# Performance work log

Hardware: AMD Instinct MI355X
Metric: run time of the kernel (lower is better)

The kernel has to match this reference:

```python
import jax, jax.numpy as jnp
import numpy as np

EPS = 1e-5
NUM_HEAD = 8
HEAD_DIM = 64
SCALE = HEAD_DIM ** -0.5


def setup_inputs() -> dict:
    key = jax.random.key(0)
    ks = jax.random.split(key, 3)
    b, n, dim = 4, 2048, 512
    inner = NUM_HEAD * HEAD_DIM  # 512
    x = jax.random.normal(ks[0], (b, n, dim), dtype=jnp.float32)
    ln_w = jnp.ones((dim,), jnp.float32)
    ln_b = jnp.zeros((dim,), jnp.float32)
    qkv_w = jax.random.normal(ks[1], (3 * inner, dim), jnp.float32) * (dim ** -0.5)
    qkv_b = jnp.zeros((3 * inner,), jnp.float32)
    out_w = jax.random.normal(ks[2], (dim, inner), jnp.float32) * (inner ** -0.5)
    out_b = jnp.zeros((dim,), jnp.float32)
    return {"x": x, "ln_w": ln_w, "ln_b": ln_b, "qkv_w": qkv_w,
            "qkv_b": qkv_b, "out_w": out_w, "out_b": out_b}


def reference(x, ln_w, ln_b, qkv_w, qkv_b, out_w, out_b):
    b, n, dim = x.shape
    # Pre-norm LayerNorm
    mu = jnp.mean(x, axis=-1, keepdims=True)
    var = jnp.mean(jnp.square(x - mu), axis=-1, keepdims=True)
    xn = (x - mu) * jax.lax.rsqrt(var + EPS) * ln_w + ln_b
    # QKV projection (torch Linear: y = x @ W.T + b)
    qkv = xn @ qkv_w.T + qkv_b  # [b, n, 3*inner]
    q, k, v = jnp.split(qkv, 3, axis=-1)
    def heads(t):  # [b, n, inner] -> [b, h, n, d]
        return t.reshape(b, n, NUM_HEAD, HEAD_DIM).transpose(0, 2, 1, 3)
    q, k, v = heads(q), heads(k), heads(v)
    # Naive full attention (materializes [b, h, n, n])
    dots = jnp.einsum('bhqd,bhkd->bhqk', q, k) * SCALE
    attn = jax.nn.softmax(dots, axis=-1)
    o = jnp.einsum('bhqk,bhkd->bhqd', attn, v)
    o = o.transpose(0, 2, 1, 3).reshape(b, n, NUM_HEAD * HEAD_DIM)
    return o @ out_w.T + out_b
```

## Files before the change

kernel.cpp:

```cpp
#include <hip/hip_runtime.h>

typedef __attribute__((ext_vector_type(8))) short bf16x8;
typedef __attribute__((ext_vector_type(4))) float floatx4;

#define B_    4
#define N_    2048
#define DIM_  512
#define NH_   8
#define HD_   64
#define SCALE_ 0.125f
#define SL2E_ (0.125f * 1.44269504f)

__device__ __forceinline__ unsigned short f32_to_bf16(float f) {
    unsigned int u = __float_as_uint(f);
    u += 0x7FFFu + ((u >> 16) & 1u);
    return (unsigned short)(u >> 16);
}

__device__ __forceinline__ float bf16_to_f32(unsigned short u) {
    return __uint_as_float(((unsigned int)u) << 16);
}

__device__ __forceinline__ floatx4 mfma16(bf16x8 a, bf16x8 b, floatx4 c) {
    return __builtin_amdgcn_mfma_f32_16x16x32_bf16(a, b, c, 0, 0, 0);
}

__device__ __forceinline__ floatx4 fzero4() {
    floatx4 z = {0.f, 0.f, 0.f, 0.f};
    return z;
}

__device__ __forceinline__ void async16(const unsigned short* g, unsigned short* l) {
    __builtin_amdgcn_global_load_lds((const __attribute__((address_space(1))) void*)g,
                                     (__attribute__((address_space(3))) void*)l,
                                     16, 0, 0);
}

__global__ __launch_bounds__(256) void ln_kernel(const float* __restrict__ x,
                                                 const float* __restrict__ w,
                                                 const float* __restrict__ b,
                                                 unsigned short* __restrict__ xn) {
    int row = blockIdx.x;
    int tid = threadIdx.x;
    int lane = tid & 63, wid = tid >> 6;
    const float2 v = ((const float2*)(x + (size_t)row * DIM_))[tid];
    float s = v.x + v.y;
    float sq = v.x * v.x + v.y * v.y;
#pragma unroll
    for (int off = 1; off < 64; off <<= 1) {
        s  += __shfl_xor(s, off, 64);
        sq += __shfl_xor(sq, off, 64);
    }
    __shared__ float red[2][4];
    if (lane == 0) { red[0][wid] = s; red[1][wid] = sq; }
    __syncthreads();
    s  = red[0][0] + red[0][1] + red[0][2] + red[0][3];
    sq = red[1][0] + red[1][1] + red[1][2] + red[1][3];
    float mu   = s * (1.f / DIM_);
    float var  = sq * (1.f / DIM_) - mu * mu;
    float rstd = rsqrtf(var + 1e-5f);
    float2 wv = ((const float2*)w)[tid];
    float2 bv = ((const float2*)b)[tid];
    float y0 = (v.x - mu) * rstd * wv.x + bv.x;
    float y1 = (v.y - mu) * rstd * wv.y + bv.y;
    unsigned int pack = (unsigned int)f32_to_bf16(y0) |
                        ((unsigned int)f32_to_bf16(y1) << 16);
    ((unsigned int*)xn)[(size_t)row * (DIM_ / 2) + tid] = pack;
}

__global__ __launch_bounds__(256) void cvt_kernel(const float* __restrict__ srcA, int na,
                                                  const float* __restrict__ srcB, int nb,
                                                  unsigned short* __restrict__ dstA,
                                                  unsigned short* __restrict__ dstB) {
    int idx = blockIdx.x * 256 + threadIdx.x;
    if (idx < na)            dstA[idx] = f32_to_bf16(srcA[idx]);
    else if (idx < na + nb)  dstB[idx - na] = f32_to_bf16(srcB[idx - na]);
}

#define GEMM_CORE(A_, B_ptr, am0, bn0)                                              \
    __shared__ unsigned short Alds[2][128][32];                                     \
    __shared__ unsigned short Blds[2][128][32];                                     \
    int tid = threadIdx.x, lane = tid & 63, wid = tid >> 6;                         \
    int l15 = lane & 15, quad = lane >> 4;                                          \
    int wmloc = (wid >> 1) * 64, wnloc = (wid & 1) * 64;                            \
    int sr = lane >> 2;                                                             \
    int sc = (lane & 3) * 8;                                                        \
    floatx4 acc[4][4];                                                              \
    _Pragma("unroll")                                                               \
    for (int i = 0; i < 4; i++)                                                     \
        _Pragma("unroll")                                                           \
        for (int j = 0; j < 4; j++) acc[i][j] = fzero4();                           \
    int buf = 0;                                                                    \
    _Pragma("unroll")                                                               \
    for (int i = 0; i < 2; i++) {                                                   \
        int r0 = 32 * wid + 16 * i;                                                 \
        async16(A_ + (size_t)(am0 + r0 + sr) * DIM_ + sc, &Alds[0][r0][0]);         \
        async16(B_ptr + (size_t)(bn0 + r0 + sr) * DIM_ + sc, &Blds[0][r0][0]);      \
    }                                                                               \
    __syncthreads();                                                                \
    for (int t = 0; t < 16; t++) {                                                  \
        if (t < 15) {                                                               \
            int k0 = (t + 1) * 32;                                                  \
            _Pragma("unroll")                                                       \
            for (int i = 0; i < 2; i++) {                                           \
                int r0 = 32 * wid + 16 * i;                                         \
                async16(A_ + (size_t)(am0 + r0 + sr) * DIM_ + k0 + sc,              \
                        &Alds[buf ^ 1][r0][0]);                                     \
                async16(B_ptr + (size_t)(bn0 + r0 + sr) * DIM_ + k0 + sc,           \
                        &Blds[buf ^ 1][r0][0]);                                     \
            }                                                                       \
        }                                                                           \
        bf16x8 av[4], bv[4];                                                        \
        _Pragma("unroll")                                                           \
        for (int i = 0; i < 4; i++)                                                 \
            av[i] = *(const bf16x8*)(&Alds[buf][wmloc + 16 * i + l15][quad * 8]);   \
        _Pragma("unroll")                                                           \
        for (int j = 0; j < 4; j++)                                                 \
            bv[j] = *(const bf16x8*)(&Blds[buf][wnloc + 16 * j + l15][quad * 8]);   \
        _Pragma("unroll")                                                           \
        for (int i = 0; i < 4; i++)                                                 \
            _Pragma("unroll")                                                       \
            for (int j = 0; j < 4; j++)                                             \
                acc[i][j] = mfma16(av[i], bv[j], acc[i][j]);                        \
        __syncthreads();                                                            \
        buf ^= 1;                                                                   \
    }

__global__ __launch_bounds__(256, 4) void qkv_gemm(const unsigned short* __restrict__ A,
                                                   const unsigned short* __restrict__ Bw,
                                                   const float* __restrict__ bias,
                                                   unsigned short* __restrict__ Qh,
                                                   unsigned short* __restrict__ Kh,
                                                   unsigned short* __restrict__ Vt) {
    int am0 = blockIdx.x * 128, bn0 = blockIdx.y * 128;
    GEMM_CORE(A, Bw, am0, bn0)

    if (bn0 >= 1024) {
        unsigned short* sc_ = &Alds[0][0][0] + wid * (16 * 68);
        int m0 = am0 + wmloc;
        int bidx = m0 >> 11;
        int t0 = m0 & 2047;
#pragma unroll
        for (int j = 0; j < 4; j++) {
            float bias_n = bias[bn0 + wnloc + 16 * j + l15];
#pragma unroll
            for (int i = 0; i < 4; i++)
#pragma unroll
                for (int r = 0; r < 4; r++)
                    sc_[l15 * 68 + 16 * i + quad * 4 + r] =
                        f32_to_bf16(acc[i][j][r] + bias_n);
#pragma unroll
            for (int half = 0; half < 2; half++) {
                int nr = 8 * half + (lane >> 3);
                int rem = (bn0 - 1024) + wnloc + 16 * j + nr;
                int head = rem >> 6, d = rem & 63;
                bf16x8 vv = *(const bf16x8*)(sc_ + nr * 68 + (lane & 7) * 8);
                *(bf16x8*)(Vt + ((size_t)(bidx * NH_ + head) * HD_ + d) * N_ +
                           t0 + (lane & 7) * 8) = vv;
            }
        }
    } else {
#pragma unroll
        for (int i = 0; i < 4; i++) {
#pragma unroll
            for (int j = 0; j < 4; j++) {
                int n = bn0 + wnloc + 16 * j + l15;
                float bias_n = bias[n];
                int which = n >> 9;
                int rem = n & 511;
                int head = rem >> 6;
                int d = rem & 63;
#pragma unroll
                for (int r = 0; r < 4; r++) {
                    int m = am0 + wmloc + 16 * i + quad * 4 + r;
                    int b = m >> 11;
                    int t = m & 2047;
                    float val = acc[i][j][r] + bias_n;
                    if (which == 0) {
                        Qh[((size_t)(b * NH_ + head) * N_ + t) * HD_ + d] =
                            f32_to_bf16(val * SL2E_);
                    } else {
                        Kh[((size_t)(b * NH_ + head) * N_ + t) * HD_ + d] =
                            f32_to_bf16(val);
                    }
                }
            }
        }
    }
}

__global__ __launch_bounds__(256, 4) void out_gemm(const unsigned short* __restrict__ A,
                                                   const unsigned short* __restrict__ Bw,
                                                   const float* __restrict__ bias,
                                                   float* __restrict__ out) {
    int am0 = blockIdx.x * 128, bn0 = blockIdx.y * 128;
    GEMM_CORE(A, Bw, am0, bn0)

#pragma unroll
    for (int i = 0; i < 4; i++) {
#pragma unroll
        for (int j = 0; j < 4; j++) {
            int n = bn0 + wnloc + 16 * j + l15;
            float bias_n = bias[n];
#pragma unroll
            for (int r = 0; r < 4; r++) {
                int m = am0 + wmloc + 16 * i + quad * 4 + r;
                out[(size_t)m * DIM_ + n] = acc[i][j][r] + bias_n;
            }
        }
    }
}

__global__ __launch_bounds__(256, 4) void attn_kernel(const unsigned short* __restrict__ Qh,
                                                      const unsigned short* __restrict__ Kh,
                                                      const unsigned short* __restrict__ Vtg,
                                                      unsigned short* __restrict__ Opart,
                                                      float* __restrict__ lpart) {
    int bh = blockIdx.y;
    int b = bh >> 3, head = bh & 7;
    int qt = blockIdx.x;
    int split = blockIdx.z;
    int kv0 = split << 10;
    int tid = threadIdx.x, lane = tid & 63, w = tid >> 6;
    int l15 = lane & 15, quad = lane >> 4;

    const unsigned short* Qp = Qh + (size_t)bh * N_ * HD_;
    const unsigned short* Kg = Kh + (size_t)bh * N_ * HD_;
    const unsigned short* Vg = Vtg + (size_t)bh * HD_ * N_;

    int q0 = qt * 128 + w * 32;

    bf16x8 aQ[2][2];
#pragma unroll
    for (int mh = 0; mh < 2; mh++) {
        const unsigned short* qrow = Qp + (size_t)(q0 + mh * 16 + l15) * HD_ + quad * 8;
        aQ[mh][0] = *(const bf16x8*)(qrow);
        aQ[mh][1] = *(const bf16x8*)(qrow + 32);
    }

    floatx4 of[2][4];
#pragma unroll
    for (int mh = 0; mh < 2; mh++)
#pragma unroll
        for (int t = 0; t < 4; t++) of[mh][t] = fzero4();
    floatx4 lacc[2];
    lacc[0] = fzero4(); lacc[1] = fzero4();

    const short onebf = (short)0x3F80;
    bf16x8 ones = {onebf, onebf, onebf, onebf, onebf, onebf, onebf, onebf};

    __shared__ unsigned short Kt[64][64];
    __shared__ unsigned short Vs[64][64];
    __shared__ unsigned short Pl[4][32][72];

    int srow = lane >> 3;
    int scol = ((lane & 7) ^ srow) * 8;

    int swz0 = (quad ^ (l15 & 7)) * 8;
    int swz1 = ((quad + 4) ^ (l15 & 7)) * 8;

    unsigned short* myP = &Pl[w][0][0];
    for (int kv = kv0; kv < kv0 + 1024; kv += 64) {
#pragma unroll
        for (int i = 0; i < 2; i++) {
            int r0 = 16 * w + 8 * i;
            async16(Kg + (size_t)(kv + r0 + srow) * HD_ + scol, &Kt[r0][0]);
            async16(Vg + (size_t)(r0 + srow) * N_ + kv + scol, &Vs[r0][0]);
        }
        __syncthreads();
        bf16x8 kf[8];
#pragma unroll
        for (int h = 0; h < 4; h++) {
            kf[2 * h]     = *(const bf16x8*)(&Kt[16 * h + l15][swz0]);
            kf[2 * h + 1] = *(const bf16x8*)(&Kt[16 * h + l15][swz1]);
        }
#pragma unroll
        for (int mh = 0; mh < 2; mh++) {
            floatx4 c[4];
#pragma unroll
            for (int h = 0; h < 4; h++) {
                floatx4 cc = fzero4();
                cc = mfma16(aQ[mh][0], kf[2 * h], cc);
                cc = mfma16(aQ[mh][1], kf[2 * h + 1], cc);
                c[h] = cc;
            }
            unsigned short* pw = myP + (mh * 16 + quad * 4) * 72 + l15;
#pragma unroll
            for (int h = 0; h < 4; h++)
#pragma unroll
                for (int r = 0; r < 4; r++)
                    pw[r * 72 + h * 16] = f32_to_bf16(exp2f(c[h][r]));
        }
        bf16x8 vf[8];
#pragma unroll
        for (int t = 0; t < 4; t++) {
            vf[2 * t]     = *(const bf16x8*)(&Vs[16 * t + l15][swz0]);
            vf[2 * t + 1] = *(const bf16x8*)(&Vs[16 * t + l15][swz1]);
        }
#pragma unroll
        for (int mh = 0; mh < 2; mh++) {
            const unsigned short* pr = myP + (mh * 16 + l15) * 72;
            bf16x8 aP0 = *(const bf16x8*)(pr + quad * 8);
            bf16x8 aP1 = *(const bf16x8*)(pr + 32 + quad * 8);
#pragma unroll
            for (int t = 0; t < 4; t++) {
                of[mh][t] = mfma16(aP0, vf[2 * t], of[mh][t]);
                of[mh][t] = mfma16(aP1, vf[2 * t + 1], of[mh][t]);
            }
            lacc[mh] = mfma16(aP0, ones, lacc[mh]);
            lacc[mh] = mfma16(aP1, ones, lacc[mh]);
        }
        __syncthreads();
    }

    unsigned short* Od = Opart + (size_t)split * B_ * N_ * DIM_;
#pragma unroll
    for (int mh = 0; mh < 2; mh++) {
        float inv[4];
#pragma unroll
        for (int r = 0; r < 4; r++) inv[r] = 1.f / lacc[mh][r];
#pragma unroll
        for (int t = 0; t < 4; t++) {
#pragma unroll
            for (int r = 0; r < 4; r++) {
                int t_tok = q0 + mh * 16 + quad * 4 + r;
                int d = 16 * t + l15;
                Od[((size_t)b * N_ + t_tok) * DIM_ + head * HD_ + d] =
                    f32_to_bf16(of[mh][t][r] * inv[r]);
            }
        }
        if (l15 == 0) {
#pragma unroll
            for (int r = 0; r < 4; r++) {
                int t_tok = q0 + mh * 16 + quad * 4 + r;
                lpart[(size_t)split * B_ * NH_ * N_ + (size_t)bh * N_ + t_tok] =
                    lacc[mh][r];
            }
        }
    }
}

__global__ __launch_bounds__(256) void combine_kernel(const unsigned short* __restrict__ Opart,
                                                      const float* __restrict__ lpart,
                                                      unsigned short* __restrict__ Obuf) {
    int idx = blockIdx.x * 256 + threadIdx.x;
    int row = idx >> 7;
    int head = (idx & 127) >> 4;
    int b = row >> 11, t = row & 2047;
    size_t li = (size_t)(b * NH_ + head) * N_ + t;
    float l1 = lpart[li];
    float l2 = lpart[(size_t)B_ * NH_ * N_ + li];
    float s = 1.f / (l1 + l2);
    float w1 = l1 * s, w2 = l2 * s;
    const size_t half = (size_t)B_ * N_ * DIM_;
    ushort4 a = ((const ushort4*)Opart)[idx];
    ushort4 c = ((const ushort4*)(Opart + half))[idx];
    ushort4 o;
    o.x = f32_to_bf16(w1 * bf16_to_f32(a.x) + w2 * bf16_to_f32(c.x));
    o.y = f32_to_bf16(w1 * bf16_to_f32(a.y) + w2 * bf16_to_f32(c.y));
    o.z = f32_to_bf16(w1 * bf16_to_f32(a.z) + w2 * bf16_to_f32(c.z));
    o.w = f32_to_bf16(w1 * bf16_to_f32(a.w) + w2 * bf16_to_f32(c.w));
    ((ushort4*)Obuf)[idx] = o;
}

extern "C" void kernel_launch(void* const* d_in, const int* in_sizes, int n_in,
                              void* d_out, int out_size, void* d_ws, size_t ws_size,
                              hipStream_t stream) {
    const float* x     = (const float*)d_in[0];
    const float* ln_w  = (const float*)d_in[1];
    const float* ln_b  = (const float*)d_in[2];
    const float* qkv_w = (const float*)d_in[3];
    const float* qkv_b = (const float*)d_in[4];
    const float* out_w = (const float*)d_in[5];
    const float* out_b = (const float*)d_in[6];
    float* out = (float*)d_out;

    char* ws = (char*)d_ws;
    const size_t TOK = (size_t)B_ * N_;
    unsigned short* xn    = (unsigned short*)ws;  ws += TOK * DIM_ * 2;
    unsigned short* wq_bf = (unsigned short*)ws;  ws += (size_t)3 * DIM_ * DIM_ * 2;
    unsigned short* wo_bf = (unsigned short*)ws;  ws += (size_t)DIM_ * DIM_ * 2;
    unsigned short* Qh    = (unsigned short*)ws;  ws += TOK * DIM_ * 2;
    unsigned short* Kh    = (unsigned short*)ws;  ws += TOK * DIM_ * 2;
    unsigned short* Vt    = (unsigned short*)ws;  ws += TOK * DIM_ * 2;
    unsigned short* Obuf  = (unsigned short*)ws;  ws += TOK * DIM_ * 2;
    unsigned short* Opart = (unsigned short*)ws;  ws += (size_t)2 * TOK * DIM_ * 2;
    float*          lpart = (float*)ws;           ws += (size_t)2 * B_ * NH_ * N_ * 4;

    const int NW = 3 * DIM_ * DIM_;
    const int NO = DIM_ * DIM_;

    ln_kernel<<<TOK, 256, 0, stream>>>(x, ln_w, ln_b, xn);
    cvt_kernel<<<(NW + NO + 255) / 256, 256, 0, stream>>>(qkv_w, NW, out_w, NO, wq_bf, wo_bf);
    qkv_gemm<<<dim3(TOK / 128, (3 * DIM_) / 128), 256, 0, stream>>>(xn, wq_bf, qkv_b, Qh, Kh, Vt);
    attn_kernel<<<dim3(N_ / 128, B_ * NH_, 2), 256, 0, stream>>>(Qh, Kh, Vt, Opart, lpart);
    combine_kernel<<<(TOK * DIM_) / 4 / 256, 256, 0, stream>>>(Opart, lpart, Obuf);
    out_gemm<<<dim3(TOK / 128, DIM_ / 128), 256, 0, stream>>>(Obuf, wo_bf, out_b, out);
}
```

Before: 183.0 us.

## Use 512-thread GEMM blocks and four-way KV split in attention

The QKV and output GEMMs move to 512-thread blocks, with each of eight waves computing a 32x64 sub-tile, so more waves are available to hide latency. The attention kernel splits the KV range into four chunks instead of two, which doubles the grid. It also processes P and V per 16-row half to shrink the P shared-memory buffer and reduce register pressure, with a higher occupancy hint. The combine kernel now merges four partials, which adds extra global traffic for Opart and lpart.

```diff
diff --git a/kernel.cpp b/kernel.cpp
--- a/kernel.cpp
+++ b/kernel.cpp
@@ -77,48 +77,41 @@
     else if (idx < na + nb)  dstB[idx - na] = f32_to_bf16(srcB[idx - na]);
 }
 
-#define GEMM_CORE(A_, B_ptr, am0, bn0)                                              \
+#define GEMM_CORE512(A_, B_ptr, am0, bn0)                                           \
     __shared__ unsigned short Alds[2][128][32];                                     \
     __shared__ unsigned short Blds[2][128][32];                                     \
     int tid = threadIdx.x, lane = tid & 63, wid = tid >> 6;                         \
     int l15 = lane & 15, quad = lane >> 4;                                          \
-    int wmloc = (wid >> 1) * 64, wnloc = (wid & 1) * 64;                            \
+    int wmloc = (wid >> 1) * 32, wnloc = (wid & 1) * 64;                            \
     int sr = lane >> 2;                                                             \
     int sc = (lane & 3) * 8;                                                        \
-    floatx4 acc[4][4];                                                              \
+    int srow0 = 16 * wid;                                                           \
+    floatx4 acc[2][4];                                                              \
     _Pragma("unroll")                                                               \
-    for (int i = 0; i < 4; i++)                                                     \
+    for (int i = 0; i < 2; i++)                                                     \
         _Pragma("unroll")                                                           \
         for (int j = 0; j < 4; j++) acc[i][j] = fzero4();                           \
     int buf = 0;                                                                    \
-    _Pragma("unroll")                                                               \
-    for (int i = 0; i < 2; i++) {                                                   \
-        int r0 = 32 * wid + 16 * i;                                                 \
-        async16(A_ + (size_t)(am0 + r0 + sr) * DIM_ + sc, &Alds[0][r0][0]);         \
-        async16(B_ptr + (size_t)(bn0 + r0 + sr) * DIM_ + sc, &Blds[0][r0][0]);      \
-    }                                                                               \
+    async16(A_ + (size_t)(am0 + srow0 + sr) * DIM_ + sc, &Alds[0][srow0][0]);       \
+    async16(B_ptr + (size_t)(bn0 + srow0 + sr) * DIM_ + sc, &Blds[0][srow0][0]);    \
     __syncthreads();                                                                \
     for (int t = 0; t < 16; t++) {                                                  \
         if (t < 15) {                                                               \
             int k0 = (t + 1) * 32;                                                  \
-            _Pragma("unroll")                                                       \
-            for (int i = 0; i < 2; i++) {                                           \
-                int r0 = 32 * wid + 16 * i;                                         \
-                async16(A_ + (size_t)(am0 + r0 + sr) * DIM_ + k0 + sc,              \
-                        &Alds[buf ^ 1][r0][0]);                                     \
-                async16(B_ptr + (size_t)(bn0 + r0 + sr) * DIM_ + k0 + sc,           \
-                        &Blds[buf ^ 1][r0][0]);                                     \
-            }                                                                       \
+            async16(A_ + (size_t)(am0 + srow0 + sr) * DIM_ + k0 + sc,               \
+                    &Alds[buf ^ 1][srow0][0]);                                      \
+            async16(B_ptr + (size_t)(bn0 + srow0 + sr) * DIM_ + k0 + sc,            \
+                    &Blds[buf ^ 1][srow0][0]);                                      \
         }                                                                           \
-        bf16x8 av[4], bv[4];                                                        \
+        bf16x8 av[2], bv[4];                                                        \
         _Pragma("unroll")                                                           \
-        for (int i = 0; i < 4; i++)                                                 \
+        for (int i = 0; i < 2; i++)                                                 \
             av[i] = *(const bf16x8*)(&Alds[buf][wmloc + 16 * i + l15][quad * 8]);   \
         _Pragma("unroll")                                                           \
         for (int j = 0; j < 4; j++)                                                 \
             bv[j] = *(const bf16x8*)(&Blds[buf][wnloc + 16 * j + l15][quad * 8]);   \
         _Pragma("unroll")                                                           \
-        for (int i = 0; i < 4; i++)                                                 \
+        for (int i = 0; i < 2; i++)                                                 \
             _Pragma("unroll")                                                       \
             for (int j = 0; j < 4; j++)                                             \
                 acc[i][j] = mfma16(av[i], bv[j], acc[i][j]);                        \
@@ -126,17 +119,17 @@
         buf ^= 1;                                                                   \
     }
 
-__global__ __launch_bounds__(256, 4) void qkv_gemm(const unsigned short* __restrict__ A,
+__global__ __launch_bounds__(512, 6) void qkv_gemm(const unsigned short* __restrict__ A,
                                                    const unsigned short* __restrict__ Bw,
                                                    const float* __restrict__ bias,
                                                    unsigned short* __restrict__ Qh,
                                                    unsigned short* __restrict__ Kh,
                                                    unsigned short* __restrict__ Vt) {
     int am0 = blockIdx.x * 128, bn0 = blockIdx.y * 128;
-    GEMM_CORE(A, Bw, am0, bn0)
+    GEMM_CORE512(A, Bw, am0, bn0)
 
     if (bn0 >= 1024) {
-        unsigned short* sc_ = &Alds[0][0][0] + wid * (16 * 68);
+        unsigned short* sc_ = &Alds[0][0][0] + wid * (16 * 40);
         int m0 = am0 + wmloc;
         int bidx = m0 >> 11;
         int t0 = m0 & 2047;
@@ -144,24 +137,21 @@
         for (int j = 0; j < 4; j++) {
             float bias_n = bias[bn0 + wnloc + 16 * j + l15];
 #pragma unroll
-            for (int i = 0; i < 4; i++)
+            for (int i = 0; i < 2; i++)
 #pragma unroll
                 for (int r = 0; r < 4; r++)
-                    sc_[l15 * 68 + 16 * i + quad * 4 + r] =
+                    sc_[l15 * 40 + 16 * i + quad * 4 + r] =
                         f32_to_bf16(acc[i][j][r] + bias_n);
-#pragma unroll
-            for (int half = 0; half < 2; half++) {
-                int nr = 8 * half + (lane >> 3);
-                int rem = (bn0 - 1024) + wnloc + 16 * j + nr;
-                int head = rem >> 6, d = rem & 63;
-                bf16x8 vv = *(const bf16x8*)(sc_ + nr * 68 + (lane & 7) * 8);
-                *(bf16x8*)(Vt + ((size_t)(bidx * NH_ + head) * HD_ + d) * N_ +
-                           t0 + (lane & 7) * 8) = vv;
-            }
+            int nr = lane >> 2;
+            int rem = (bn0 - 1024) + wnloc + 16 * j + nr;
+            int head = rem >> 6, d = rem & 63;
+            bf16x8 vv = *(const bf16x8*)(sc_ + nr * 40 + (lane & 3) * 8);
+            *(bf16x8*)(Vt + ((size_t)(bidx * NH_ + head) * HD_ + d) * N_ +
+                       t0 + (lane & 3) * 8) = vv;
         }
     } else {
 #pragma unroll
-        for (int i = 0; i < 4; i++) {
+        for (int i = 0; i < 2; i++) {
 #pragma unroll
             for (int j = 0; j < 4; j++) {
                 int n = bn0 + wnloc + 16 * j + l15;
@@ -189,15 +179,15 @@
     }
 }
 
-__global__ __launch_bounds__(256, 4) void out_gemm(const unsigned short* __restrict__ A,
+__global__ __launch_bounds__(512, 4) void out_gemm(const unsigned short* __restrict__ A,
                                                    const unsigned short* __restrict__ Bw,
                                                    const float* __restrict__ bias,
                                                    float* __restrict__ out) {
     int am0 = blockIdx.x * 128, bn0 = blockIdx.y * 128;
-    GEMM_CORE(A, Bw, am0, bn0)
-
-#pragma unroll
-    for (int i = 0; i < 4; i++) {
+    GEMM_CORE512(A, Bw, am0, bn0)
+
+#pragma unroll
+    for (int i = 0; i < 2; i++) {
 #pragma unroll
         for (int j = 0; j < 4; j++) {
             int n = bn0 + wnloc + 16 * j + l15;
@@ -211,7 +201,7 @@
     }
 }
 
-__global__ __launch_bounds__(256, 4) void attn_kernel(const unsigned short* __restrict__ Qh,
+__global__ __launch_bounds__(256, 6) void attn_kernel(const unsigned short* __restrict__ Qh,
                                                       const unsigned short* __restrict__ Kh,
                                                       const unsigned short* __restrict__ Vtg,
                                                       unsigned short* __restrict__ Opart,
@@ -220,7 +210,7 @@
     int b = bh >> 3, head = bh & 7;
     int qt = blockIdx.x;
     int split = blockIdx.z;
-    int kv0 = split << 10;
+    int kv0 = split << 9;
     int tid = threadIdx.x, lane = tid & 63, w = tid >> 6;
     int l15 = lane & 15, quad = lane >> 4;
 
@@ -251,7 +241,7 @@
 
     __shared__ unsigned short Kt[64][64];
     __shared__ unsigned short Vs[64][64];
-    __shared__ unsigned short Pl[4][32][72];
+    __shared__ unsigned short Pl[4][16][72];
 
     int srow = lane >> 3;
     int scol = ((lane & 7) ^ srow) * 8;
@@ -260,7 +250,7 @@
     int swz1 = ((quad + 4) ^ (l15 & 7)) * 8;
 
     unsigned short* myP = &Pl[w][0][0];
-    for (int kv = kv0; kv < kv0 + 1024; kv += 64) {
+    for (int kv = kv0; kv < kv0 + 512; kv += 64) {
 #pragma unroll
         for (int i = 0; i < 2; i++) {
             int r0 = 16 * w + 8 * i;
@@ -284,28 +274,21 @@
                 cc = mfma16(aQ[mh][1], kf[2 * h + 1], cc);
                 c[h] = cc;
             }
-            unsigned short* pw = myP + (mh * 16 + quad * 4) * 72 + l15;
+            unsigned short* pw = myP + (quad * 4) * 72 + l15;
 #pragma unroll
             for (int h = 0; h < 4; h++)
 #pragma unroll
                 for (int r = 0; r < 4; r++)
                     pw[r * 72 + h * 16] = f32_to_bf16(exp2f(c[h][r]));
-        }
-        bf16x8 vf[8];
-#pragma unroll
-        for (int t = 0; t < 4; t++) {
-            vf[2 * t]     = *(const bf16x8*)(&Vs[16 * t + l15][swz0]);
-            vf[2 * t + 1] = *(const bf16x8*)(&Vs[16 * t + l15][swz1]);
-        }
-#pragma unroll
-        for (int mh = 0; mh < 2; mh++) {
-            const unsigned short* pr = myP + (mh * 16 + l15) * 72;
+            const unsigned short* pr = myP + l15 * 72;
             bf16x8 aP0 = *(const bf16x8*)(pr + quad * 8);
             bf16x8 aP1 = *(const bf16x8*)(pr + 32 + quad * 8);
 #pragma unroll
             for (int t = 0; t < 4; t++) {
-                of[mh][t] = mfma16(aP0, vf[2 * t], of[mh][t]);
-                of[mh][t] = mfma16(aP1, vf[2 * t + 1], of[mh][t]);
+                bf16x8 v0 = *(const bf16x8*)(&Vs[16 * t + l15][swz0]);
+                bf16x8 v1 = *(const bf16x8*)(&Vs[16 * t + l15][swz1]);
+                of[mh][t] = mfma16(aP0, v0, of[mh][t]);
+                of[mh][t] = mfma16(aP1, v1, of[mh][t]);
             }
             lacc[mh] = mfma16(aP0, ones, lacc[mh]);
             lacc[mh] = mfma16(aP1, ones, lacc[mh]);
@@ -333,8 +316,7 @@
 #pragma unroll
             for (int r = 0; r < 4; r++) {
                 int t_tok = q0 + mh * 16 + quad * 4 + r;
-                lpart[(size_t)split * B_ * NH_ * N_ + (size_t)bh * N_ + t_tok] =
-                    lacc[mh][r];
+                lpart[((size_t)split * B_ * NH_ + bh) * N_ + t_tok] = lacc[mh][r];
             }
         }
     }
@@ -348,18 +330,27 @@
     int head = (idx & 127) >> 4;
     int b = row >> 11, t = row & 2047;
     size_t li = (size_t)(b * NH_ + head) * N_ + t;
-    float l1 = lpart[li];
-    float l2 = lpart[(size_t)B_ * NH_ * N_ + li];
-    float s = 1.f / (l1 + l2);
-    float w1 = l1 * s, w2 = l2 * s;
-    const size_t half = (size_t)B_ * N_ * DIM_;
-    ushort4 a = ((const ushort4*)Opart)[idx];
-    ushort4 c = ((const ushort4*)(Opart + half))[idx];
+    const size_t LSTRIDE = (size_t)B_ * NH_ * N_;
+    const size_t OSTRIDE = (size_t)B_ * N_ * DIM_;
+    float l[4];
+#pragma unroll
+    for (int s = 0; s < 4; s++) l[s] = lpart[s * LSTRIDE + li];
+    float inv = 1.f / (l[0] + l[1] + l[2] + l[3]);
+    float acc0 = 0.f, acc1 = 0.f, acc2 = 0.f, acc3 = 0.f;
+#pragma unroll
+    for (int s = 0; s < 4; s++) {
+        float ws = l[s] * inv;
+        ushort4 a = ((const ushort4*)(Opart + s * OSTRIDE))[idx];
+        acc0 += ws * bf16_to_f32(a.x);
+        acc1 += ws * bf16_to_f32(a.y);
+        acc2 += ws * bf16_to_f32(a.z);
+        acc3 += ws * bf16_to_f32(a.w);
+    }
     ushort4 o;
-    o.x = f32_to_bf16(w1 * bf16_to_f32(a.x) + w2 * bf16_to_f32(c.x));
-    o.y = f32_to_bf16(w1 * bf16_to_f32(a.y) + w2 * bf16_to_f32(c.y));
-    o.z = f32_to_bf16(w1 * bf16_to_f32(a.z) + w2 * bf16_to_f32(c.z));
-    o.w = f32_to_bf16(w1 * bf16_to_f32(a.w) + w2 * bf16_to_f32(c.w));
+    o.x = f32_to_bf16(acc0);
+    o.y = f32_to_bf16(acc1);
+    o.z = f32_to_bf16(acc2);
+    o.w = f32_to_bf16(acc3);
     ((ushort4*)Obuf)[idx] = o;
 }
 
@@ -384,16 +375,16 @@
     unsigned short* Kh    = (unsigned short*)ws;  ws += TOK * DIM_ * 2;
     unsigned short* Vt    = (unsigned short*)ws;  ws += TOK * DIM_ * 2;
     unsigned short* Obuf  = (unsigned short*)ws;  ws += TOK * DIM_ * 2;
-    unsigned short* Opart = (unsigned short*)ws;  ws += (size_t)2 * TOK * DIM_ * 2;
-    float*          lpart = (float*)ws;           ws += (size_t)2 * B_ * NH_ * N_ * 4;
+    unsigned short* Opart = (unsigned short*)ws;  ws += (size_t)4 * TOK * DIM_ * 2;
+    float*          lpart = (float*)ws;           ws += (size_t)4 * B_ * NH_ * N_ * 4;
 
     const int NW = 3 * DIM_ * DIM_;
     const int NO = DIM_ * DIM_;
 
     ln_kernel<<<TOK, 256, 0, stream>>>(x, ln_w, ln_b, xn);
     cvt_kernel<<<(NW + NO + 255) / 256, 256, 0, stream>>>(qkv_w, NW, out_w, NO, wq_bf, wo_bf);
-    qkv_gemm<<<dim3(TOK / 128, (3 * DIM_) / 128), 256, 0, stream>>>(xn, wq_bf, qkv_b, Qh, Kh, Vt);
-    attn_kernel<<<dim3(N_ / 128, B_ * NH_, 2), 256, 0, stream>>>(Qh, Kh, Vt, Opart, lpart);
+    qkv_gemm<<<dim3(TOK / 128, (3 * DIM_) / 128), 512, 0, stream>>>(xn, wq_bf, qkv_b, Qh, Kh, Vt);
+    attn_kernel<<<dim3(N_ / 128, B_ * NH_, 4), 256, 0, stream>>>(Qh, Kh, Vt, Opart, lpart);
     combine_kernel<<<(TOK * DIM_) / 4 / 256, 256, 0, stream>>>(Opart, lpart, Obuf);
-    out_gemm<<<dim3(TOK / 128, DIM_ / 128), 256, 0, stream>>>(Obuf, wo_bf, out_b, out);
-}
+    out_gemm<<<dim3(TOK / 128, DIM_ / 128), 512, 0, stream>>>(Obuf, wo_bf, out_b, out);
+}
```

Result: slower. 342.7 us (+87.2%).
